# Optimization experiments

Hardware: AMD Instinct MI355X
Metric: run time of the kernel (lower is better)

The kernel has to match this reference:

```python
import jax, jax.numpy as jnp
import numpy as np

ALPHA = 0.2          # LeakyReLU negative slope
ORTHO_LAMBDA = 0.01  # orthogonal regularization weight


def setup_inputs() -> dict:
    key = jax.random.key(0)
    ks = jax.random.split(key, 9)
    N, IN, OUT, NR, H = 50000, 128, 128, 64, 4
    E1, E2 = 200000, 50000
    return {
        "input": jax.random.normal(ks[0], (N, IN), jnp.float32),
        "edge": jax.random.randint(ks[1], (2, E1), 0, N),
        "edge_embed": jax.random.normal(ks[2], (E1, NR), jnp.float32),
        "edge_list_nhop": jax.random.randint(ks[3], (2, E2), 0, N),
        "edge_embed_nhop": jax.random.normal(ks[4], (E2, NR), jnp.float32),
        "proj": jax.random.normal(ks[5], (H, IN, IN), jnp.float32) / np.sqrt(IN).astype(np.float32),
        "W": jax.random.normal(ks[6], (H, OUT, 2 * IN + NR), jnp.float32) * 0.08,
        "a": jax.random.normal(ks[7], (H, 1, OUT), jnp.float32) * 0.1,
        "head_weights": jnp.ones((H,), jnp.float32),
    }


def reference(input, edge, edge_embed, edge_list_nhop, edge_embed_nhop, proj, W, a, head_weights):
    N, IN = input.shape
    H, OUT, _ = W.shape
    e = jnp.concatenate([edge, edge_list_nhop], axis=1)              # [2, E]
    emb = jnp.concatenate([edge_embed, edge_embed_nhop], axis=0)     # [E, NR]
    src, tgt = e[0], e[1]

    # per-head orthogonal projections: head_input[h] = input @ proj[h].T -> [H, N, IN]
    hin = jnp.einsum('ni,hoi->hno', input, proj)

    # edge_m = W @ concat(h_src, h_tgt, rel) without materializing the concat
    W_src, W_tgt, W_rel = W[:, :, :IN], W[:, :, IN:2 * IN], W[:, :, 2 * IN:]
    edge_m = (jnp.einsum('hei,hoi->heo', hin[:, src, :], W_src)
              + jnp.einsum('hei,hoi->heo', hin[:, tgt, :], W_tgt)
              + jnp.einsum('er,hor->heo', emb, W_rel))               # [H, E, OUT]

    scores = jnp.einsum('heo,ho->he', edge_m, a[:, 0, :])            # [H, E]
    powers = -jnp.where(scores > 0, scores, ALPHA * scores)         # -leakyrelu
    edge_e = jnp.exp(powers)                                         # [H, E]

    seg = lambda v: jax.ops.segment_sum(v, src, num_segments=N)
    e_rowsum = jnp.clip(jax.vmap(seg)(edge_e), 1e-12, None)          # [H, N]

    edge_w = edge_e[:, :, None] * edge_m                             # [H, E, OUT]
    head_out = jax.vmap(seg)(edge_w)                                 # [H, N, OUT]

    w = jax.nn.softmax(head_weights)
    out = jnp.einsum('h,hnd->nd', w, head_out)                       # [N, OUT]
    # faithful to torch: divides by the LAST head's e_rowsum (loop leakage)
    out = out / e_rowsum[-1][:, None]

    pp = jnp.einsum('hij,hkj->hik', proj, proj)                      # proj @ proj.T
    eye = jnp.eye(proj.shape[1], dtype=proj.dtype)
    orth_reg = ORTHO_LAMBDA * jnp.sum(jnp.sqrt(jnp.sum((pp - eye) ** 2, axis=(1, 2))))

    return jax.nn.elu(out), orth_reg
```

## Files before the change

### kernel.cpp

```cpp
#include <hip/hip_runtime.h>
#include <math.h>


#define NHEAD 4

typedef unsigned short u16;
typedef __attribute__((ext_vector_type(4))) unsigned short u16x4;
typedef __attribute__((ext_vector_type(8))) unsigned short u16x8;
typedef __attribute__((ext_vector_type(8))) short bf16x8;
typedef __attribute__((ext_vector_type(4))) float f32x4;

__device__ __forceinline__ float bf2f(u16 v) {
    union { unsigned u; float f; } x; x.u = ((unsigned)v) << 16; return x.f;
}
__device__ __forceinline__ u16 f2bf(float f) {
    union { float f; unsigned u; } x; x.f = f;
    const unsigned r = x.u + 0x7FFFu + ((x.u >> 16) & 1u);
    return (u16)(r >> 16);
}

__global__ __launch_bounds__(256) void k1_prep(
    const float* __restrict__ proj, const float* __restrict__ W,
    const float* __restrict__ a, const float* __restrict__ hw,
    u16* __restrict__ M_bf,
    float* __restrict__ asrc, float* __restrict__ atgt, float* __restrict__ arel,
    u16* __restrict__ WcatT_bf, float* __restrict__ wsoft,
    float* __restrict__ orth_part)
{
    __shared__ float projS[128*132];
    __shared__ float WS[32*132];
    __shared__ float tS[128];
    __shared__ float red[256];
    const int h = blockIdx.x;
    const int part = blockIdx.y;
    const int z = blockIdx.z;
    const int tid = threadIdx.x;
    if (part < 2 && z >= 4) return;
    const float* projH = proj + h*(128*128);
    const float* WH = W + h*(128*320);
    const float* aH = a + h*128;

    {
        const float4* p4 = (const float4*)projH;
        for (int idx = tid; idx < 4096; idx += 256)
            *(float4*)&projS[(idx>>5)*132 + (idx&31)*4] = p4[idx];
    }

    if (part < 2) {
        const int koff = part ? 128 : 0;
        for (int idx = tid; idx < 1024; idx += 256) {
            const int ol = idx>>5, jq = idx&31;
            *(float4*)&WS[ol*132 + jq*4] = *(const float4*)&WH[(z*32+ol)*320 + koff + jq*4];
        }
        __syncthreads();
        u16* Mout = M_bf + ((size_t)(part*4 + h))*16384;
        for (int idx = tid; idx < 1024; idx += 256) {
            const int ol = idx>>5, jq = idx&31;
            float4 acc; acc.x=0.f; acc.y=0.f; acc.z=0.f; acc.w=0.f;
            for (int i = 0; i < 128; ++i) {
                const float wv = WS[ol*132 + i];
                const float4 pv = *(const float4*)&projS[i*132 + jq*4];
                acc.x += wv*pv.x; acc.y += wv*pv.y; acc.z += wv*pv.z; acc.w += wv*pv.w;
            }
            u16x4 pk; pk.x=f2bf(acc.x); pk.y=f2bf(acc.y); pk.z=f2bf(acc.z); pk.w=f2bf(acc.w);
            *(u16x4*)&Mout[(z*32+ol)*128 + jq*4] = pk;
        }
        if (z == 0) {
            if (tid < 128) {
                float s = 0.f;
                for (int o = 0; o < 128; ++o) s += aH[o]*WH[o*320 + koff + tid];
                tS[tid] = s;
            }
            __syncthreads();
            if (tid < 128) {
                float s = 0.f;
                for (int i = 0; i < 128; ++i) s += tS[i]*projS[i*132 + tid];
                (part ? atgt : asrc)[h*128 + tid] = s;
            }
        }
    } else {
        __syncthreads();
        float local = 0.f;
        const int base = z*2048;
        for (int idx = base + tid; idx < base + 2048; idx += 256) {
            const int i = idx>>7, k = idx&127;
            if (i > k) continue;
            float s = 0.f;
            for (int q = 0; q < 32; ++q) {
                const float4 pi = *(const float4*)&projS[i*132 + q*4];
                const float4 pk = *(const float4*)&projS[k*132 + q*4];
                s += pi.x*pk.x + pi.y*pk.y + pi.z*pk.z + pi.w*pk.w;
            }
            if (i == k) { s -= 1.f; local += s*s; }
            else local += 2.f*s*s;
        }
        red[tid] = local;
        __syncthreads();
        for (int st = 128; st > 0; st >>= 1) {
            if (tid < st) red[tid] += red[tid+st];
            __syncthreads();
        }
        if (tid == 0) atomicAdd(&orth_part[h], red[0]);
        if (z == 0) {
            if (tid < 64) {
                float s = 0.f;
                for (int o = 0; o < 128; ++o) s += aH[o]*WH[o*320 + 256 + tid];
                arel[h*64 + tid] = s;
            }
            for (int idx = tid; idx < 8192; idx += 256) {
                const int r = idx & 63, o = idx >> 6;
                WcatT_bf[(size_t)o*256 + h*64 + r] = f2bf(WH[o*320 + 256 + r]);
            }
            if (h == 0 && tid == 0) {
                const float m = fmaxf(fmaxf(hw[0],hw[1]), fmaxf(hw[2],hw[3]));
                const float e0=expf(hw[0]-m), e1=expf(hw[1]-m), e2=expf(hw[2]-m), e3=expf(hw[3]-m);
                const float s = e0+e1+e2+e3;
                wsoft[0]=e0/s; wsoft[1]=e1/s; wsoft[2]=e2/s; wsoft[3]=e3/s;
            }
        }
    }
}

__global__ __launch_bounds__(256) void k0_nodes(
    const float* __restrict__ input, const float* __restrict__ asrc, const float* __restrict__ atgt,
    u16* __restrict__ in_bf, float* __restrict__ s_src, float* __restrict__ s_tgt, int N)
{
    __shared__ float aS[512], tS[512];
    const int tid = threadIdx.x;
    for (int idx = tid; idx < 512; idx += 256) { aS[idx] = asrc[idx]; tS[idx] = atgt[idx]; }
    __syncthreads();
    const int n = blockIdx.x*256 + tid;
    if (n >= N) return;
    const float4* inr = (const float4*)(input + (size_t)n*128);
    u16* ob = in_bf + (size_t)n*128;
    float ss[4] = {0.f,0.f,0.f,0.f}, st[4] = {0.f,0.f,0.f,0.f};
    for (int q = 0; q < 32; ++q) {
        const float4 v = inr[q];
        u16x4 pk; pk.x=f2bf(v.x); pk.y=f2bf(v.y); pk.z=f2bf(v.z); pk.w=f2bf(v.w);
        *(u16x4*)(ob + q*4) = pk;
        #pragma unroll
        for (int hh = 0; hh < 4; ++hh) {
            const float4 av = *(const float4*)&aS[hh*128 + q*4];
            const float4 tv = *(const float4*)&tS[hh*128 + q*4];
            ss[hh] += v.x*av.x + v.y*av.y + v.z*av.z + v.w*av.w;
            st[hh] += v.x*tv.x + v.y*tv.y + v.z*tv.z + v.w*tv.w;
        }
    }
    float4 o1; o1.x=ss[0]; o1.y=ss[1]; o1.z=ss[2]; o1.w=ss[3];
    float4 o2; o2.x=st[0]; o2.y=st[1]; o2.z=st[2]; o2.w=st[3];
    *(float4*)(s_src + (size_t)n*4) = o1;
    *(float4*)(s_tgt + (size_t)n*4) = o2;
}

__global__ __launch_bounds__(256) void k2_mfma(
    const u16* __restrict__ in_bf, const u16* __restrict__ M_bf,
    u16* __restrict__ tbl, int N)
{
    __shared__ u16 MS[16384];
    __shared__ u16 DW[4][16*136];
    const int tid = threadIdx.x;
    const int w = tid >> 6, lane = tid & 63;
    const int bid = blockIdx.x;
    const int nx = gridDim.x >> 3;
    const int swz = (bid & 7)*nx + (bid >> 3);
    const int n0 = (swz >> 3)*256;
    const int mat = swz & 7;
    const int m = lane & 15, kg = lane >> 4;

    {
        const u16* Mp = M_bf + (size_t)mat*16384;
        for (int c = tid; c < 2048; c += 256) {
            const int row = c >> 4, c16 = c & 15;
            const u16x8 v = *(const u16x8*)(Mp + row*128 + c16*8);
            *(u16x8*)((char*)MS + row*256 + ((c16*16) ^ ((row&7)<<4))) = v;
        }
    }
    __syncthreads();

    bf16x8 fa[8][4];
    #pragma unroll
    for (int nt = 0; nt < 8; ++nt) {
        const int row = nt*16 + m;
        #pragma unroll
        for (int ks = 0; ks < 4; ++ks) {
            const int c16 = ks*4 + kg;
            fa[nt][ks] = *(const bf16x8*)((const char*)MS + row*256 + ((c16*16) ^ ((row&7)<<4)));
        }
    }

    for (int sub = 0; sub < 4; ++sub) {
        const int nrow = n0 + w*64 + sub*16 + m;
        const int nclamp = (nrow < N) ? nrow : (N-1);
        bf16x8 fb[4];
        #pragma unroll
        for (int ks = 0; ks < 4; ++ks)
            fb[ks] = *(const bf16x8*)(in_bf + (size_t)nclamp*128 + ks*32 + kg*8);
        f32x4 acc[8];
        #pragma unroll
        for (int nt = 0; nt < 8; ++nt) { acc[nt][0]=0.f; acc[nt][1]=0.f; acc[nt][2]=0.f; acc[nt][3]=0.f; }
        #pragma unroll
        for (int nt = 0; nt < 8; ++nt)
            #pragma unroll
            for (int ks = 0; ks < 4; ++ks)
                acc[nt] = __builtin_amdgcn_mfma_f32_16x16x32_bf16(fa[nt][ks], fb[ks], acc[nt], 0, 0, 0);
        #pragma unroll
        for (int nt = 0; nt < 8; ++nt) {
            unsigned lo, hi;
            asm("v_cvt_pk_bf16_f32 %0, %1, %2" : "=v"(lo) : "v"(acc[nt][0]), "v"(acc[nt][1]));
            asm("v_cvt_pk_bf16_f32 %0, %1, %2" : "=v"(hi) : "v"(acc[nt][2]), "v"(acc[nt][3]));
            uint2 pk; pk.x = lo; pk.y = hi;
            *(uint2*)&DW[w][m*136 + nt*16 + kg*4] = pk;
        }
        __syncthreads();
        const int nb = n0 + w*64 + sub*16;
        #pragma unroll
        for (int k = 0; k < 4; ++k) {
            const int idx = lane + k*64;
            const int row = idx >> 4, seg = idx & 15;
            const int n = nb + row;
            if (n < N) {
                const bf16x8 v = *(const bf16x8*)&DW[w][row*136 + seg*8];
                *(bf16x8*)(tbl + (size_t)n*1024 + mat*128 + seg*8) = v;
            }
        }
        __syncthreads();
    }
}

__global__ __launch_bounds__(256) void k_deg(
    const int* __restrict__ edge, const int* __restrict__ nhop,
    int* __restrict__ deg, int E1, int E2)
{
    const int e = blockIdx.x*256 + threadIdx.x;
    if (e >= E1+E2) return;
    const int src = (e < E1) ? edge[e] : nhop[e-E1];
    atomicAdd(&deg[src], 1);
}

__global__ __launch_bounds__(1024) void k_scanA(const int* __restrict__ deg, int* __restrict__ offsets,
                                                int* __restrict__ bsum, int N)
{
    __shared__ int wsumS[16];
    const int tid = threadIdx.x;
    const int lane = tid & 63, wid = tid >> 6;
    const int i0 = blockIdx.x*4096 + tid*4;
    int a0=0,a1=0,a2=0,a3=0;
    if (i0 + 3 < N) { const int4 t = *(const int4*)(deg + i0); a0=t.x; a1=t.y; a2=t.z; a3=t.w; }
    else { if (i0 < N) a0=deg[i0]; if (i0+1 < N) a1=deg[i0+1]; if (i0+2 < N) a2=deg[i0+2]; }
    const int s1=a0+a1, s2=s1+a2, s3=s2+a3;
    int s = s3;
    #pragma unroll
    for (int d = 1; d < 64; d <<= 1) { const int t = __shfl_up(s, d); if (lane >= d) s += t; }
    if (lane == 63) wsumS[wid] = s;
    __syncthreads();
    if (tid < 16) {
        int t = wsumS[tid];
        #pragma unroll
        for (int d = 1; d < 16; d <<= 1) { const int u = __shfl_up(t, d); if (tid >= d) t += u; }
        wsumS[tid] = t;
    }
    __syncthreads();
    const int ex = (wid ? wsumS[wid-1] : 0) + s - s3;
    if (i0 < N)     offsets[i0]   = ex;
    if (i0+1 < N)   offsets[i0+1] = ex + a0;
    if (i0+2 < N)   offsets[i0+2] = ex + s1;
    if (i0+3 < N)   offsets[i0+3] = ex + s2;
    if (tid == 0) bsum[blockIdx.x] = wsumS[15];
}

__global__ __launch_bounds__(64) void k_scanB(const int* __restrict__ bsum, int* __restrict__ boff,
                                              int* __restrict__ offsets, int nb, int N)
{
    const int tid = threadIdx.x;
    const int v = (tid < nb) ? bsum[tid] : 0;
    int s = v;
    #pragma unroll
    for (int d = 1; d < 64; d <<= 1) { const int t = __shfl_up(s, d); if (tid >= d) s += t; }
    if (tid < nb) boff[tid] = s - v;
    if (tid == 63) offsets[N] = s;
}

__global__ __launch_bounds__(256) void k_fill2(
    const int* __restrict__ edge, const int* __restrict__ nhop,
    const float* __restrict__ emb1, const float* __restrict__ emb2,
    const float* __restrict__ s_src, const float* __restrict__ s_tgt,
    const float* __restrict__ arel,
    const int* __restrict__ offsets, const int* __restrict__ boff, int* __restrict__ cursor,
    int* __restrict__ csr_tgt, float* __restrict__ ee_perm, u16* __restrict__ emb_perm,
    int E1, int E2)
{
    const int tid = threadIdx.x;
    const int g = tid >> 4, l = tid & 15;
    const int E = E1 + E2;
    const float4 ar0 = *(const float4*)(arel + 0*64 + l*4);
    const float4 ar1 = *(const float4*)(arel + 1*64 + l*4);
    const float4 ar2 = *(const float4*)(arel + 2*64 + l*4);
    const float4 ar3 = *(const float4*)(arel + 3*64 + l*4);
    const int ebase = blockIdx.x*256;
    #pragma unroll 4
    for (int it = 0; it < 16; ++it) {
        const int e = ebase + it*16 + g;
        if (e >= E) continue;
        const float4 v = (e < E1) ? *(const float4*)(emb1 + (size_t)e*64 + l*4)
                                  : *(const float4*)(emb2 + (size_t)(e-E1)*64 + l*4);
        u16x4 pk; pk.x=f2bf(v.x); pk.y=f2bf(v.y); pk.z=f2bf(v.z); pk.w=f2bf(v.w);
        float p0 = v.x*ar0.x + v.y*ar0.y + v.z*ar0.z + v.w*ar0.w;
        float p1 = v.x*ar1.x + v.y*ar1.y + v.z*ar1.z + v.w*ar1.w;
        float p2 = v.x*ar2.x + v.y*ar2.y + v.z*ar2.z + v.w*ar2.w;
        float p3 = v.x*ar3.x + v.y*ar3.y + v.z*ar3.z + v.w*ar3.w;
        #pragma unroll
        for (int d = 1; d < 16; d <<= 1) {
            p0 += __shfl_xor(p0, d);
            p1 += __shfl_xor(p1, d);
            p2 += __shfl_xor(p2, d);
            p3 += __shfl_xor(p3, d);
        }
        int p = 0;
        if (l == 0) {
            int src, tgt;
            if (e < E1) { src = edge[e]; tgt = edge[E1+e]; }
            else { const int e2 = e-E1; src = nhop[e2]; tgt = nhop[E2+e2]; }
            const float4 s4 = *(const float4*)(s_src + (size_t)src*4);
            const float4 t4 = *(const float4*)(s_tgt + (size_t)tgt*4);
            float4 eo;
            { const float sc = s4.x+t4.x+p0; eo.x = expf(sc>0.f ? -sc : -0.2f*sc); }
            { const float sc = s4.y+t4.y+p1; eo.y = expf(sc>0.f ? -sc : -0.2f*sc); }
            { const float sc = s4.z+t4.z+p2; eo.z = expf(sc>0.f ? -sc : -0.2f*sc); }
            { const float sc = s4.w+t4.w+p3; eo.w = expf(sc>0.f ? -sc : -0.2f*sc); }
            const int pos = atomicAdd(&cursor[src], 1);
            p = offsets[src] + boff[src>>12] + pos;
            csr_tgt[p] = tgt;
            *(float4*)(ee_perm + (size_t)p*4) = eo;
        }
        p = __shfl(p, tid & 48);
        *(u16x4*)(emb_perm + (size_t)p*64 + l*4) = pk;
    }
}

__global__ __launch_bounds__(256) void k4_gather(
    const float* __restrict__ ee_perm, const int* __restrict__ offsets, const int* __restrict__ boff,
    const int* __restrict__ csr_tgt,
    const u16* __restrict__ emb_perm, const u16* __restrict__ tbl,
    const float* __restrict__ wsoft,
    u16* __restrict__ pout_bf, u16* __restrict__ semb_bf, float* __restrict__ rowsum3,
    int N)
{
    __shared__ float eeS[4][64][4];
    __shared__ int   tgS[4][64];
    const int lane = threadIdx.x & 63;
    const int wv = threadIdx.x >> 6;
    const int n = blockIdx.x*4 + wv;
    if (n >= N) return;
    const int hl = lane >> 4;
    const int hoff = hl*128 + (lane & 15)*8;

    union HT { u16x8 v; unsigned u[4]; };

    float acc[8];
    #pragma unroll
    for (int j = 0; j < 8; ++j) acc[j] = 0.f;
    float sm0=0.f, sm1=0.f, sm2=0.f, sm3=0.f;
    float rsl0=0.f, rsl1=0.f, rsl2=0.f, rsl3=0.f;

    const int start = offsets[n] + boff[n>>12];
    const int end = (n+1 == N) ? offsets[N] : (offsets[n+1] + boff[(n+1)>>12]);
    for (int cb = start; cb < end; cb += 64) {
        const int rem = end - cb;
        const int cnt = rem < 64 ? rem : 64;
        int tgtL = 0;
        float4 eeL; eeL.x=0.f; eeL.y=0.f; eeL.z=0.f; eeL.w=0.f;
        if (lane < cnt) {
            tgtL = csr_tgt[cb + lane];
            eeL  = *(const float4*)(ee_perm + (size_t)(cb + lane)*4);
        }
        rsl0 += eeL.x; rsl1 += eeL.y; rsl2 += eeL.z; rsl3 += eeL.w;
        *(float4*)&eeS[wv][lane][0] = eeL;
        tgS[wv][lane] = tgtL;
        const int cp = (cnt + 3) & ~3;

        HT zz; zz.u[0]=0u; zz.u[1]=0u; zz.u[2]=0u; zz.u[3]=0u;
        HT ht0=zz, ht1=zz, ht2=zz, ht3=zz;
        u16 em0=0, em1=0, em2=0, em3=0;
#define K4_FETCH(J, IDX) { const int tg_ = tgS[wv][IDX]; \
            ht##J.v = *(const u16x8*)(tbl + (size_t)tg_*1024 + 512 + hoff); \
            em##J = emb_perm[(size_t)(cb + (IDX))*64 + lane]; }
        if (0 < cnt) K4_FETCH(0, 0)
        if (1 < cnt) K4_FETCH(1, 1)
        if (2 < cnt) K4_FETCH(2, 2)
        if (3 < cnt) K4_FETCH(3, 3)

#define K4_STAGE(J) { \
            const float4 ee4 = *(const float4*)&eeS[wv][i+J][0]; \
            const float eh = eeS[wv][i+J][hl]; \
            _Pragma("unroll") \
            for (int p = 0; p < 4; ++p) { \
                union{unsigned u; float f;} lo_, hi_; \
                lo_.u = ht##J.u[p] << 16; hi_.u = ht##J.u[p] & 0xffff0000u; \
                acc[2*p]   += eh*lo_.f; \
                acc[2*p+1] += eh*hi_.f; \
            } \
            const float ev = bf2f(em##J); \
            sm0 += ee4.x*ev; sm1 += ee4.y*ev; sm2 += ee4.z*ev; sm3 += ee4.w*ev; \
            { const int ii = i + 4 + J; if (ii < cnt) K4_FETCH(J, ii) } }

        for (int i = 0; i < cp; i += 4) {
            K4_STAGE(0)
            K4_STAGE(1)
            K4_STAGE(2)
            K4_STAGE(3)
        }
#undef K4_STAGE
#undef K4_FETCH
    }

    #pragma unroll
    for (int d = 1; d < 64; d <<= 1) {
        rsl0 += __shfl_xor(rsl0, d);
        rsl1 += __shfl_xor(rsl1, d);
        rsl2 += __shfl_xor(rsl2, d);
        rsl3 += __shfl_xor(rsl3, d);
    }
    {
        const float rsh = (hl==0)?rsl0:(hl==1)?rsl1:(hl==2)?rsl2:rsl3;
        HT hs; hs.v = *(const u16x8*)(tbl + (size_t)n*1024 + hoff);
        #pragma unroll
        for (int p = 0; p < 4; ++p) {
            union{unsigned u; float f;} lo_, hi_;
            lo_.u = hs.u[p] << 16; hi_.u = hs.u[p] & 0xffff0000u;
            acc[2*p]   += rsh*lo_.f;
            acc[2*p+1] += rsh*hi_.f;
        }
    }
    if (lane == 0) rowsum3[n] = fmaxf(rsl3, 1e-12f);

    const float4 ws4 = *(const float4*)wsoft;
    const float wh = (hl==0)?ws4.x:(hl==1)?ws4.y:(hl==2)?ws4.z:ws4.w;
    float p[8];
    #pragma unroll
    for (int j = 0; j < 8; ++j) {
        float pv = wh*acc[j];
        pv += __shfl_xor(pv, 16);
        pv += __shfl_xor(pv, 32);
        p[j] = pv;
    }
    if (hl == 0) {
        u16 pk[8];
        #pragma unroll
        for (int j = 0; j < 8; ++j) pk[j] = f2bf(p[j]);
        *(u16x8*)(pout_bf + (size_t)n*128 + (lane & 15)*8) = *(u16x8*)pk;
    }
    u16* so = semb_bf + (size_t)n*256;
    so[lane]       = f2bf(ws4.x*sm0);
    so[64 + lane]  = f2bf(ws4.y*sm1);
    so[128 + lane] = f2bf(ws4.z*sm2);
    so[192 + lane] = f2bf(ws4.w*sm3);
}

__global__ __launch_bounds__(256) void k5_gemm(
    const u16* __restrict__ semb_bf, const u16* __restrict__ wcatT_bf,
    const u16* __restrict__ pout_bf,
    const float* __restrict__ rowsum3, const float* __restrict__ orth_part,
    float* __restrict__ out, int N)
{
    __shared__ float DS[64*132];
    const int tid = threadIdx.x;
    if (blockIdx.x == 0 && tid == 0)
        out[(size_t)N*128] = 0.01f*(sqrtf(orth_part[0])+sqrtf(orth_part[1])+sqrtf(orth_part[2])+sqrtf(orth_part[3]));
    const int w = tid >> 6, lane = tid & 63;
    const int m = lane & 15, kg = lane >> 4;
    const int n0 = blockIdx.x*64;

    bf16x8 fa[8];
    {
        int row = n0 + w*16 + m; if (row >= N) row = N-1;
        const u16* ap = semb_bf + (size_t)row*256 + kg*8;
        #pragma unroll
        for (int ks = 0; ks < 8; ++ks) fa[ks] = *(const bf16x8*)(ap + ks*32);
    }
    f32x4 acc[8];
    #pragma unroll
    for (int nt = 0; nt < 8; ++nt) { acc[nt][0]=0.f; acc[nt][1]=0.f; acc[nt][2]=0.f; acc[nt][3]=0.f; }
    #pragma unroll
    for (int nt = 0; nt < 8; ++nt) {
        const u16* bp = wcatT_bf + (size_t)(nt*16 + m)*256 + kg*8;
        #pragma unroll
        for (int ks = 0; ks < 8; ++ks) {
            const bf16x8 fb = *(const bf16x8*)(bp + ks*32);
            acc[nt] = __builtin_amdgcn_mfma_f32_16x16x32_bf16(fa[ks], fb, acc[nt], 0, 0, 0);
        }
    }
    #pragma unroll
    for (int nt = 0; nt < 8; ++nt) {
        const int o = nt*16 + m;
        const int r0 = w*16 + kg*4;
        #pragma unroll
        for (int r = 0; r < 4; ++r)
            DS[(r0+r)*132 + o] = acc[nt][r];
    }
    __syncthreads();
    for (int idx = tid; idx < 2048; idx += 256) {
        const int row = idx >> 5, q = idx & 31;
        const int n = n0 + row;
        if (n < N) {
            const float4 d = *(const float4*)&DS[row*132 + q*4];
            const u16x4 pb = *(const u16x4*)(pout_bf + (size_t)n*128 + q*4);
            const float rinv = 1.0f / rowsum3[n];
            float v0 = (bf2f(pb.x) + d.x)*rinv;
            float v1 = (bf2f(pb.y) + d.y)*rinv;
            float v2 = (bf2f(pb.z) + d.z)*rinv;
            float v3 = (bf2f(pb.w) + d.w)*rinv;
            v0 = (v0 > 0.f) ? v0 : expm1f(v0);
            v1 = (v1 > 0.f) ? v1 : expm1f(v1);
            v2 = (v2 > 0.f) ? v2 : expm1f(v2);
            v3 = (v3 > 0.f) ? v3 : expm1f(v3);
            float4 r4; r4.x=v0; r4.y=v1; r4.z=v2; r4.w=v3;
            *(float4*)(out + (size_t)n*128 + q*4) = r4;
        }
    }
}

extern "C" void kernel_launch(void* const* d_in, const int* in_sizes, int n_in,
                              void* d_out, int out_size, void* d_ws, size_t ws_size,
                              hipStream_t stream)
{
    const float* input = (const float*)d_in[0];
    const int*   edge  = (const int*)d_in[1];
    const float* emb1  = (const float*)d_in[2];
    const int*   nhop  = (const int*)d_in[3];
    const float* emb2  = (const float*)d_in[4];
    const float* proj  = (const float*)d_in[5];
    const float* W     = (const float*)d_in[6];
    const float* a     = (const float*)d_in[7];
    const float* hw    = (const float*)d_in[8];
    float* out = (float*)d_out;

    const int N  = in_sizes[0] / 128;
    const int E1 = in_sizes[1] / 2;
    const int E2 = in_sizes[3] / 2;
    const int E  = E1 + E2;
    (void)n_in; (void)out_size; (void)ws_size;

    char* wsb = (char*)d_ws;
    size_t off = 0;
    auto alloc = [&](size_t bytes) -> char* {
        char* p = wsb + off;
        off += (bytes + 255) & ~(size_t)255;
        return p;
    };
    u16*   in_bf    = (u16*)alloc((size_t)N*128*2);
    u16*   tbl      = (u16*)alloc((size_t)N*1024*2);
    u16*   semb_bf  = (u16*)alloc((size_t)N*256*2);
    u16*   pout_bf  = (u16*)alloc((size_t)N*128*2);
    u16*   emb_perm = (u16*)alloc((size_t)E*64*2);
    float* ee_perm  = (float*)alloc((size_t)E*4*4);
    int*   csr_tgt  = (int*)alloc((size_t)E*4);
    u16*   M_bf     = (u16*)alloc((size_t)8*16384*2);
    u16*   WcatT_bf = (u16*)alloc((size_t)128*256*2);
    float* asrc     = (float*)alloc(512*4);
    float* atgt     = (float*)alloc(512*4);
    float* arel     = (float*)alloc(256*4);
    float* s_src    = (float*)alloc((size_t)N*4*4);
    float* s_tgt    = (float*)alloc((size_t)N*4*4);
    float* wsoft    = (float*)alloc(4*4);
    float* rowsum3  = (float*)alloc((size_t)N*4);
    int*   offsets  = (int*)alloc((size_t)(N+1)*4);
    int*   bsum     = (int*)alloc(64*4);
    int*   boff     = (int*)alloc(64*4);
    const size_t zoff0 = off;
    float* orth_part= (float*)alloc(4*4);
    int*   deg      = (int*)alloc((size_t)N*4);
    int*   cursor   = (int*)alloc((size_t)N*4);
    const size_t zoff1 = off;

    hipMemsetAsync(wsb + zoff0, 0, zoff1 - zoff0, stream);

    const int nbScan = (N + 4095) / 4096;
    const int nx = (N + 255) / 256;

    k1_prep<<<dim3(NHEAD,3,8), dim3(256), 0, stream>>>(proj, W, a, hw, M_bf,
                                                       asrc, atgt, arel, WcatT_bf, wsoft, orth_part);
    k0_nodes<<<dim3((N+255)/256), dim3(256), 0, stream>>>(input, asrc, atgt, in_bf, s_src, s_tgt, N);
    k2_mfma<<<dim3(nx*8), dim3(256), 0, stream>>>(in_bf, M_bf, tbl, N);
    k_deg<<<dim3((E+255)/256), dim3(256), 0, stream>>>(edge, nhop, deg, E1, E2);
    k_scanA<<<dim3(nbScan), dim3(1024), 0, stream>>>(deg, offsets, bsum, N);
    k_scanB<<<dim3(1), dim3(64), 0, stream>>>(bsum, boff, offsets, nbScan, N);
    k_fill2<<<dim3((E+255)/256), dim3(256), 0, stream>>>(edge, nhop, emb1, emb2, s_src, s_tgt,
                                                         arel, offsets, boff, cursor,
                                                         csr_tgt, ee_perm, emb_perm, E1, E2);
    k4_gather<<<dim3((N+3)/4), dim3(256), 0, stream>>>(ee_perm, offsets, boff, csr_tgt, emb_perm,
                                                       tbl, wsoft, pout_bf, semb_bf, rowsum3, N);
    k5_gemm<<<dim3((N+63)/64), dim3(256), 0, stream>>>(semb_bf, WcatT_bf, pout_bf, rowsum3, orth_part,
                                                       out, N);
}
```

Measured before the change: 257.6 us.

## Fuse degree count into node kernel, drop MFMA syncs, grid-stride gather

Folds the per-edge degree atomic count into the node conversion kernel, which removes one launch. Removes the block barriers around the per-wave LDS staging in the MFMA table kernel. Makes the gather kernel grid-stride over nodes with a capped grid and cuts its prefetch depth from 4 to 2 edges, aiming to lower register pressure and launch overhead. The depth and sync changes risk less latency hiding, and possible LDS hazards if cross-lane visibility within a wave is not guaranteed.

```diff
diff --git a/kernel.cpp b/kernel.cpp
--- a/kernel.cpp
+++ b/kernel.cpp
@@ -123,13 +123,20 @@
 
 __global__ __launch_bounds__(256) void k0_nodes(
     const float* __restrict__ input, const float* __restrict__ asrc, const float* __restrict__ atgt,
-    u16* __restrict__ in_bf, float* __restrict__ s_src, float* __restrict__ s_tgt, int N)
+    const int* __restrict__ edge, const int* __restrict__ nhop,
+    u16* __restrict__ in_bf, float* __restrict__ s_src, float* __restrict__ s_tgt,
+    int* __restrict__ deg, int N, int E1, int E2)
 {
     __shared__ float aS[512], tS[512];
     const int tid = threadIdx.x;
     for (int idx = tid; idx < 512; idx += 256) { aS[idx] = asrc[idx]; tS[idx] = atgt[idx]; }
+    const int t = blockIdx.x*256 + tid;
+    if (t < E1 + E2) {
+        const int src = (t < E1) ? edge[t] : nhop[t-E1];
+        atomicAdd(&deg[src], 1);
+    }
     __syncthreads();
-    const int n = blockIdx.x*256 + tid;
+    const int n = t;
     if (n >= N) return;
     const float4* inr = (const float4*)(input + (size_t)n*128);
     u16* ob = in_bf + (size_t)n*128;
@@ -211,7 +218,6 @@
             uint2 pk; pk.x = lo; pk.y = hi;
             *(uint2*)&DW[w][m*136 + nt*16 + kg*4] = pk;
         }
-        __syncthreads();
         const int nb = n0 + w*64 + sub*16;
         #pragma unroll
         for (int k = 0; k < 4; ++k) {
@@ -223,18 +229,7 @@
                 *(bf16x8*)(tbl + (size_t)n*1024 + mat*128 + seg*8) = v;
             }
         }
-        __syncthreads();
-    }
-}
-
-__global__ __launch_bounds__(256) void k_deg(
-    const int* __restrict__ edge, const int* __restrict__ nhop,
-    int* __restrict__ deg, int E1, int E2)
-{
-    const int e = blockIdx.x*256 + threadIdx.x;
-    if (e >= E1+E2) return;
-    const int src = (e < E1) ? edge[e] : nhop[e-E1];
-    atomicAdd(&deg[src], 1);
+    }
 }
 
 __global__ __launch_bounds__(1024) void k_scanA(const int* __restrict__ deg, int* __restrict__ offsets,
@@ -349,12 +344,14 @@
     __shared__ int   tgS[4][64];
     const int lane = threadIdx.x & 63;
     const int wv = threadIdx.x >> 6;
-    const int n = blockIdx.x*4 + wv;
-    if (n >= N) return;
     const int hl = lane >> 4;
     const int hoff = hl*128 + (lane & 15)*8;
+    const int stride = gridDim.x*4;
+    const float4 ws4 = *(const float4*)wsoft;
 
     union HT { u16x8 v; unsigned u[4]; };
+
+    for (int n = blockIdx.x*4 + wv; n < N; n += stride) {
 
     float acc[8];
     #pragma unroll
@@ -376,18 +373,16 @@
         rsl0 += eeL.x; rsl1 += eeL.y; rsl2 += eeL.z; rsl3 += eeL.w;
         *(float4*)&eeS[wv][lane][0] = eeL;
         tgS[wv][lane] = tgtL;
-        const int cp = (cnt + 3) & ~3;
+        const int cp = (cnt + 1) & ~1;
 
         HT zz; zz.u[0]=0u; zz.u[1]=0u; zz.u[2]=0u; zz.u[3]=0u;
-        HT ht0=zz, ht1=zz, ht2=zz, ht3=zz;
-        u16 em0=0, em1=0, em2=0, em3=0;
+        HT ht0=zz, ht1=zz;
+        u16 em0=0, em1=0;
 #define K4_FETCH(J, IDX) { const int tg_ = tgS[wv][IDX]; \
             ht##J.v = *(const u16x8*)(tbl + (size_t)tg_*1024 + 512 + hoff); \
             em##J = emb_perm[(size_t)(cb + (IDX))*64 + lane]; }
         if (0 < cnt) K4_FETCH(0, 0)
         if (1 < cnt) K4_FETCH(1, 1)
-        if (2 < cnt) K4_FETCH(2, 2)
-        if (3 < cnt) K4_FETCH(3, 3)
 
 #define K4_STAGE(J) { \
             const float4 ee4 = *(const float4*)&eeS[wv][i+J][0]; \
@@ -401,13 +396,11 @@
             } \
             const float ev = bf2f(em##J); \
             sm0 += ee4.x*ev; sm1 += ee4.y*ev; sm2 += ee4.z*ev; sm3 += ee4.w*ev; \
-            { const int ii = i + 4 + J; if (ii < cnt) K4_FETCH(J, ii) } }
-
-        for (int i = 0; i < cp; i += 4) {
+            { const int ii = i + 2 + J; if (ii < cnt) K4_FETCH(J, ii) } }
+
+        for (int i = 0; i < cp; i += 2) {
             K4_STAGE(0)
             K4_STAGE(1)
-            K4_STAGE(2)
-            K4_STAGE(3)
         }
 #undef K4_STAGE
 #undef K4_FETCH
@@ -433,7 +426,6 @@
     }
     if (lane == 0) rowsum3[n] = fmaxf(rsl3, 1e-12f);
 
-    const float4 ws4 = *(const float4*)wsoft;
     const float wh = (hl==0)?ws4.x:(hl==1)?ws4.y:(hl==2)?ws4.z:ws4.w;
     float p[8];
     #pragma unroll
@@ -454,6 +446,8 @@
     so[64 + lane]  = f2bf(ws4.y*sm1);
     so[128 + lane] = f2bf(ws4.z*sm2);
     so[192 + lane] = f2bf(ws4.w*sm3);
+
+    }
 }
 
 __global__ __launch_bounds__(256) void k5_gemm(
@@ -576,19 +570,21 @@
 
     const int nbScan = (N + 4095) / 4096;
     const int nx = (N + 255) / 256;
+    const int nk0 = ((E > N ? E : N) + 255) / 256;
+    int nb4 = (N + 3) / 4; if (nb4 > 2048) nb4 = 2048;
 
     k1_prep<<<dim3(NHEAD,3,8), dim3(256), 0, stream>>>(proj, W, a, hw, M_bf,
                                                        asrc, atgt, arel, WcatT_bf, wsoft, orth_part);
-    k0_nodes<<<dim3((N+255)/256), dim3(256), 0, stream>>>(input, asrc, atgt, in_bf, s_src, s_tgt, N);
+    k0_nodes<<<dim3(nk0), dim3(256), 0, stream>>>(input, asrc, atgt, edge, nhop,
+                                                  in_bf, s_src, s_tgt, deg, N, E1, E2);
     k2_mfma<<<dim3(nx*8), dim3(256), 0, stream>>>(in_bf, M_bf, tbl, N);
-    k_deg<<<dim3((E+255)/256), dim3(256), 0, stream>>>(edge, nhop, deg, E1, E2);
     k_scanA<<<dim3(nbScan), dim3(1024), 0, stream>>>(deg, offsets, bsum, N);
     k_scanB<<<dim3(1), dim3(64), 0, stream>>>(bsum, boff, offsets, nbScan, N);
     k_fill2<<<dim3((E+255)/256), dim3(256), 0, stream>>>(edge, nhop, emb1, emb2, s_src, s_tgt,
                                                          arel, offsets, boff, cursor,
                                                          csr_tgt, ee_perm, emb_perm, E1, E2);
-    k4_gather<<<dim3((N+3)/4), dim3(256), 0, stream>>>(ee_perm, offsets, boff, csr_tgt, emb_perm,
-                                                       tbl, wsoft, pout_bf, semb_bf, rowsum3, N);
+    k4_gather<<<dim3(nb4), dim3(256), 0, stream>>>(ee_perm, offsets, boff, csr_tgt, emb_perm,
+                                                   tbl, wsoft, pout_bf, semb_bf, rowsum3, N);
     k5_gemm<<<dim3((N+63)/64), dim3(256), 0, stream>>>(semb_bf, WcatT_bf, pout_bf, rowsum3, orth_part,
                                                        out, N);
 }
```

Result: faster. 250.6 us (-2.7%).
